# Performance work log

Hardware: AMD Instinct MI355X
Metric: run time of the kernel (lower is better)

The kernel has to match this reference:

```python
import jax, jax.numpy as jnp
import numpy as np


def conv1x1(x, w, b):
    # x: [B,Cin,H,W], w: [Cout,Cin], b: [Cout]
    return jnp.einsum('bchw,oc->bohw', x, w) + b[None, :, None, None]


def setup_inputs() -> dict:
    key = jax.random.key(0)
    ks = jax.random.split(key, 10)
    B, Cm, C, H, W = 4, 6, 64, 64, 64
    map1 = jax.random.normal(ks[0], (B, Cm, H, W), jnp.float32)
    map2 = jax.random.normal(ks[1], (B, Cm, H, W), jnp.float32)
    feature_map = jax.random.normal(ks[2], (B, C, H, W), jnp.float32)
    # 1x1 conv params (kaiming-ish scale)
    wb = jax.random.normal(ks[3], (Cm, Cm), jnp.float32) / np.sqrt(Cm)
    bb = jnp.zeros((Cm,), jnp.float32)
    wc = jax.random.normal(ks[4], (Cm, Cm), jnp.float32) / np.sqrt(Cm)
    bc = jnp.zeros((Cm,), jnp.float32)
    wd = jax.random.normal(ks[5], (C, C), jnp.float32) / np.sqrt(C)
    bd = jnp.zeros((C,), jnp.float32)
    alpha = jnp.zeros((1,), jnp.float32)
    return {"map1": map1, "map2": map2, "feature_map": feature_map,
            "wb": wb, "bb": bb, "wc": wc, "bc": bc, "wd": wd, "bd": bd,
            "alpha": alpha}


def reference(map1, map2, feature_map, wb, bb, wc, bc, wd, bd, alpha):
    B, _, H, W = map1.shape
    N = H * W
    # conv1x1 projections, flatten spatial
    feat_b = conv1x1(map1, wb, bb).reshape(B, -1, N).transpose(0, 2, 1)  # [B,N,6]
    feat_c = conv1x1(map2, wc, bc).reshape(B, -1, N)                      # [B,6,N]
    attention_s = jax.nn.softmax(jnp.einsum('bnc,bcm->bnm', feat_b, feat_c), axis=-1)  # [B,N,N]
    feat_d = conv1x1(feature_map, wd, bd).reshape(B, -1, N)               # [B,C,N]
    # bmm with attention_s^T: out[b,c,n] = sum_m feat_d[b,c,m] * attn[b,n,m]
    feat_e = jnp.einsum('bcm,bnm->bcn', feat_d, attention_s).reshape(B, -1, H, W)
    return alpha * feat_e + feature_map
```

## Files before the change

### kernel.cpp

```cpp
#include <hip/hip_runtime.h>
#include <hip/hip_bf16.h>
#include <math.h>


#define BATCH 4
#define CMAP  6
#define CH    64
#define NSP   4096
#define TN    64
#define NTW   16
#define PSTR  72

typedef __attribute__((ext_vector_type(8))) short short8;
typedef __attribute__((ext_vector_type(4))) float f32x4;

#if __has_builtin(__builtin_amdgcn_exp2f)
#define EXP2(x) __builtin_amdgcn_exp2f(x)
#else
#define EXP2(x) exp2f(x)
#endif

__device__ __forceinline__ unsigned f2bf(float f) {
    unsigned u = __float_as_uint(f);
    return (u + 0x7fffu + ((u >> 16) & 1u)) >> 16;
}

#define INVLN2 1.44269504088896f
#define SHIFT_BF16 0xC238u
#define ONE_BF16   0x3F80u


__global__ void proj_kernel(const float* __restrict__ map1, const float* __restrict__ map2,
                            const float* __restrict__ fm,
                            const float* __restrict__ wb, const float* __restrict__ bb,
                            const float* __restrict__ wc, const float* __restrict__ bc,
                            const float* __restrict__ wd, const float* __restrict__ bd,
                            unsigned short* __restrict__ featq8,
                            unsigned short* __restrict__ featk8,
                            unsigned short* __restrict__ featdf)
{
    __shared__ unsigned short vfrag[2048];

    const int b    = blockIdx.z;
    const int half = blockIdx.y;
    const int lane = threadIdx.x & 63;
    const int og   = threadIdx.x >> 6;
    const int n    = blockIdx.x * 64 + lane;

    const int ht = lane >> 5;
    const int mm = lane & 31;
    const int q4 = mm >> 3, jj = mm & 7;
    const int cb_local = og >> 1;
    float vals[CH];
#pragma unroll
    for (int c = 0; c < CH; ++c)
        vals[c] = fm[(size_t)(b*CH + c)*NSP + n];
#pragma unroll
    for (int oi = 0; oi < 8; ++oi) {
        const int o = half*32 + og*8 + oi;
        float a = bd[o];
#pragma unroll
        for (int c = 0; c < CH; ++c)
            a = fmaf(vals[c], wd[o*CH + c], a);
        const int r = (og & 1)*8 + oi;
        vfrag[(ht*2 + cb_local)*512 + (q4*16 + r)*8 + jj] = (unsigned short)f2bf(a);
    }

    if (half == 0 && og == 0) {
        float v1[CMAP], v2[CMAP];
#pragma unroll
        for (int c = 0; c < CMAP; ++c) {
            v1[c] = map1[(size_t)(b*CMAP + c)*NSP + n];
            v2[c] = map2[(size_t)(b*CMAP + c)*NSP + n];
        }
        unsigned qv[CMAP], kv[CMAP];
#pragma unroll
        for (int o = 0; o < CMAP; ++o) {
            float a1 = bb[o], a2 = bc[o];
#pragma unroll
            for (int c = 0; c < CMAP; ++c) {
                a1 = fmaf(v1[c], wb[o*CMAP + c], a1);
                a2 = fmaf(v2[c], wc[o*CMAP + c], a2);
            }
            qv[o] = f2bf(a1 * INVLN2);
            kv[o] = f2bf(a2);
        }
        uint4 qw, kw;
        qw.x = qv[0] | (qv[1] << 16);
        qw.y = qv[2] | (qv[3] << 16);
        qw.z = qv[4] | (qv[5] << 16);
        qw.w = SHIFT_BF16;
        kw.x = kv[0] | (kv[1] << 16);
        kw.y = kv[2] | (kv[3] << 16);
        kw.z = kv[4] | (kv[5] << 16);
        kw.w = ONE_BF16;
        *(uint4*)&featq8[(size_t)(b*NSP + n)*8] = qw;
        *(uint4*)&featk8[(size_t)(b*NSP + n)*8] = kw;
    }

    __syncthreads();

    {
        const int tt = threadIdx.x;
        const uint4 d = *(const uint4*)&vfrag[tt*8];
        const int ht2 = tt >> 7, inner = tt & 127;
        const size_t off = (((size_t)(b*128 + blockIdx.x*2 + ht2)*4) + half*2)*512
                         + (size_t)inner*8;
        *(uint4*)&featdf[off] = d;
    }
}

__global__ __launch_bounds__(256, 4)
void attn_kernel(const unsigned short* __restrict__ featq8,
                 const unsigned short* __restrict__ featk8,
                 const unsigned short* __restrict__ featdf,
                 const float* __restrict__ fm, const float* __restrict__ alpha_p,
                 float* __restrict__ out)
{
    __shared__ unsigned short p_scr[2][4][16*PSTR];
    __shared__ float cmb[3][64][20];

    const int b    = blockIdx.y;
    const int t    = threadIdx.x;
    const int lane = t & 63, w = t >> 6;
    const int row16 = lane & 15, quad = lane >> 4;
    const int n0   = blockIdx.x * 16;
    const int m0   = w * (NSP/4);

    short8 qf = {0,0,0,0,0,0,0,0};
    if (quad == 0)
        qf = *(const short8*)&featq8[(size_t)(b*NSP + n0 + row16)*8];

    const short8 onesb = {(short)ONE_BF16,(short)ONE_BF16,(short)ONE_BF16,(short)ONE_BF16,
                          (short)ONE_BF16,(short)ONE_BF16,(short)ONE_BF16,(short)ONE_BF16};

    const unsigned short* kbase = featk8 + ((size_t)(b*NSP + m0) + row16)*8 + quad*8;
    const unsigned short* vfb = featdf + ((size_t)b*128*4)*512 + lane*8;
    const int hb = w * 32;

    const f32x4 zf = {0.f,0.f,0.f,0.f};
    f32x4 acc[4] = {zf, zf, zf, zf};
    f32x4 accL = zf;
    const int prow = row16 * PSTR;

#define PAM_DO(pwp, mb, sv)                                                     \
    {                                                                           \
        const float p0 = EXP2(sv[0]), p1 = EXP2(sv[1]);                         \
        const float p2 = EXP2(sv[2]), p3 = EXP2(sv[3]);                         \
        uint2 pp;                                                               \
        pp.x = __builtin_amdgcn_perm(__float_as_uint(p1), __float_as_uint(p0), 0x07060302u); \
        pp.y = __builtin_amdgcn_perm(__float_as_uint(p3), __float_as_uint(p2), 0x07060302u); \
        *(uint2*)((pwp) + (mb)*16) = pp;                                        \
    }

#define LOADK(mt)                                                               \
    kc0 = *(const short8*)(kbase + ((mt)*TN +  0)*8);                           \
    kc1 = *(const short8*)(kbase + ((mt)*TN + 16)*8);                           \
    kc2 = *(const short8*)(kbase + ((mt)*TN + 32)*8);                           \
    kc3 = *(const short8*)(kbase + ((mt)*TN + 48)*8);

#define LOADV(vt)                                                               \
    vv0 = *(const short8*)(vfb + (size_t)((hb + (vt)*2 + 0)*4 + 0)*512);        \
    vv1 = *(const short8*)(vfb + (size_t)((hb + (vt)*2 + 1)*4 + 0)*512);        \
    vv2 = *(const short8*)(vfb + (size_t)((hb + (vt)*2 + 0)*4 + 1)*512);        \
    vv3 = *(const short8*)(vfb + (size_t)((hb + (vt)*2 + 1)*4 + 1)*512);        \
    vv4 = *(const short8*)(vfb + (size_t)((hb + (vt)*2 + 0)*4 + 2)*512);        \
    vv5 = *(const short8*)(vfb + (size_t)((hb + (vt)*2 + 1)*4 + 2)*512);        \
    vv6 = *(const short8*)(vfb + (size_t)((hb + (vt)*2 + 1)*4 + 3)*512);        \
    vv7 = *(const short8*)(vfb + (size_t)((hb + (vt)*2 + 0)*4 + 3)*512);

#define PV(a0_, a1_)                                                            \
    acc[0] = __builtin_amdgcn_mfma_f32_16x16x32_bf16(a0_, vv0, acc[0], 0, 0, 0); \
    acc[0] = __builtin_amdgcn_mfma_f32_16x16x32_bf16(a1_, vv1, acc[0], 0, 0, 0); \
    acc[1] = __builtin_amdgcn_mfma_f32_16x16x32_bf16(a0_, vv2, acc[1], 0, 0, 0); \
    acc[1] = __builtin_amdgcn_mfma_f32_16x16x32_bf16(a1_, vv3, acc[1], 0, 0, 0); \
    acc[2] = __builtin_amdgcn_mfma_f32_16x16x32_bf16(a0_, vv4, acc[2], 0, 0, 0); \
    acc[2] = __builtin_amdgcn_mfma_f32_16x16x32_bf16(a1_, vv5, acc[2], 0, 0, 0); \
    acc[3] = __builtin_amdgcn_mfma_f32_16x16x32_bf16(a0_, vv7, acc[3], 0, 0, 0); \
    acc[3] = __builtin_amdgcn_mfma_f32_16x16x32_bf16(a1_, vv6, acc[3], 0, 0, 0); \
    accL   = __builtin_amdgcn_mfma_f32_16x16x32_bf16(a0_, onesb, accL, 0, 0, 0); \
    accL   = __builtin_amdgcn_mfma_f32_16x16x32_bf16(a1_, onesb, accL, 0, 0, 0);

    short8 kc0, kc1, kc2, kc3;
    short8 vv0, vv1, vv2, vv3, vv4, vv5, vv6, vv7;
    f32x4 sp0, sp1, sp2, sp3;

    LOADK(0)
    {
        f32x4 a0 = __builtin_amdgcn_mfma_f32_16x16x32_bf16(kc0, qf, zf, 0, 0, 0);
        f32x4 a1 = __builtin_amdgcn_mfma_f32_16x16x32_bf16(kc1, qf, zf, 0, 0, 0);
        f32x4 a2 = __builtin_amdgcn_mfma_f32_16x16x32_bf16(kc2, qf, zf, 0, 0, 0);
        f32x4 a3 = __builtin_amdgcn_mfma_f32_16x16x32_bf16(kc3, qf, zf, 0, 0, 0);
        LOADK(1)
        unsigned short* pw = &p_scr[0][w][prow + quad*4];
        PAM_DO(pw, 0, a0) PAM_DO(pw, 1, a1) PAM_DO(pw, 2, a2) PAM_DO(pw, 3, a3)
    }
    sp0 = __builtin_amdgcn_mfma_f32_16x16x32_bf16(kc0, qf, zf, 0, 0, 0);
    sp1 = __builtin_amdgcn_mfma_f32_16x16x32_bf16(kc1, qf, zf, 0, 0, 0);
    sp2 = __builtin_amdgcn_mfma_f32_16x16x32_bf16(kc2, qf, zf, 0, 0, 0);
    sp3 = __builtin_amdgcn_mfma_f32_16x16x32_bf16(kc3, qf, zf, 0, 0, 0);
    LOADK(2)
    LOADV(0)

#pragma unroll 2
    for (int i = 2; i < NTW; ++i) {
        const f32x4 t0 = __builtin_amdgcn_mfma_f32_16x16x32_bf16(kc0, qf, zf, 0, 0, 0);
        const f32x4 t1 = __builtin_amdgcn_mfma_f32_16x16x32_bf16(kc1, qf, zf, 0, 0, 0);
        const f32x4 t2 = __builtin_amdgcn_mfma_f32_16x16x32_bf16(kc2, qf, zf, 0, 0, 0);
        const f32x4 t3 = __builtin_amdgcn_mfma_f32_16x16x32_bf16(kc3, qf, zf, 0, 0, 0);

        LOADK(i + 1)

        const unsigned short* pr = &p_scr[i & 1][w][prow + quad*8];
        const short8 a0 = *(const short8*)pr;
        const short8 a1 = *(const short8*)(pr + 32);

        {
            unsigned short* pw = &p_scr[(i + 1) & 1][w][prow + quad*4];
            PAM_DO(pw, 0, sp0) PAM_DO(pw, 1, sp1) PAM_DO(pw, 2, sp2) PAM_DO(pw, 3, sp3)
        }

        PV(a0, a1)

        LOADV(i - 1)

        sp0 = t0; sp1 = t1; sp2 = t2; sp3 = t3;
    }

    {
        const unsigned short* pr = &p_scr[0][w][prow + quad*8];
        const short8 a0 = *(const short8*)pr;
        const short8 a1 = *(const short8*)(pr + 32);
        unsigned short* pw = &p_scr[1][w][prow + quad*4];
        PAM_DO(pw, 0, sp0) PAM_DO(pw, 1, sp1) PAM_DO(pw, 2, sp2) PAM_DO(pw, 3, sp3)
        PV(a0, a1)
        LOADV(15)
    }
    {
        const unsigned short* pr = &p_scr[1][w][prow + quad*8];
        const short8 a0 = *(const short8*)pr;
        const short8 a1 = *(const short8*)(pr + 32);
        PV(a0, a1)
    }
#undef PAM_DO
#undef LOADK
#undef LOADV
#undef PV

    if (w != 0) {
        float* c = cmb[w - 1][lane];
#pragma unroll
        for (int cb = 0; cb < 4; ++cb)
            *(float4*)&c[cb*4] = (float4){acc[cb][0], acc[cb][1], acc[cb][2], acc[cb][3]};
        *(float4*)&c[16] = (float4){accL[0], accL[1], accL[2], accL[3]};
    }
    __syncthreads();
    if (w == 0) {
#pragma unroll
        for (int ww = 0; ww < 3; ++ww) {
            const float* c = cmb[ww][lane];
#pragma unroll
            for (int cb = 0; cb < 4; ++cb) {
                const float4 po = *(const float4*)&c[cb*4];
                acc[cb][0] += po.x; acc[cb][1] += po.y;
                acc[cb][2] += po.z; acc[cb][3] += po.w;
            }
            const float4 lo = *(const float4*)&c[16];
            accL[0] += lo.x; accL[1] += lo.y; accL[2] += lo.z; accL[3] += lo.w;
        }
        const float alpha = alpha_p[0];
        const float c0 = alpha / (accL[0] + 1e-30f);
        const float c1 = alpha / (accL[1] + 1e-30f);
        const float c2 = alpha / (accL[2] + 1e-30f);
        const float c3 = alpha / (accL[3] + 1e-30f);
#pragma unroll
        for (int cb = 0; cb < 4; ++cb) {
            const int ch = cb*16 + row16;
            const size_t base = (size_t)(b*CH + ch)*NSP + n0 + quad*4;
            const float4 f = *(const float4*)&fm[base];
            float4 o;
            o.x = fmaf(c0, acc[cb][0], f.x);
            o.y = fmaf(c1, acc[cb][1], f.y);
            o.z = fmaf(c2, acc[cb][2], f.z);
            o.w = fmaf(c3, acc[cb][3], f.w);
            *(float4*)&out[base] = o;
        }
    }
}

extern "C" void kernel_launch(void* const* d_in, const int* in_sizes, int n_in,
                              void* d_out, int out_size, void* d_ws, size_t ws_size,
                              hipStream_t stream)
{
    const float* map1  = (const float*)d_in[0];
    const float* map2  = (const float*)d_in[1];
    const float* fm    = (const float*)d_in[2];
    const float* wb    = (const float*)d_in[3];
    const float* bb    = (const float*)d_in[4];
    const float* wc    = (const float*)d_in[5];
    const float* bc    = (const float*)d_in[6];
    const float* wd    = (const float*)d_in[7];
    const float* bd    = (const float*)d_in[8];
    const float* alpha = (const float*)d_in[9];
    float* out = (float*)d_out;

    unsigned short* featq8 = (unsigned short*)d_ws;
    unsigned short* featk8 = featq8 + (size_t)BATCH*NSP*8;
    unsigned short* featdf = featk8 + (size_t)BATCH*NSP*8;

    proj_kernel<<<dim3(NSP/64, 2, BATCH), 256, 0, stream>>>(
        map1, map2, fm, wb, bb, wc, bc, wd, bd, featq8, featk8, featdf);
    attn_kernel<<<dim3(NSP/16, BATCH), 256, 0, stream>>>(
        featq8, featk8, featdf, fm, alpha, out);
}
```

Measured before the change: 122.1 us.

## Split attention blocks across channel halves and query pairs instead of key quarters

Reorganizes the attention kernel so each block covers 32 queries and one half of the 64 output channels, selected by a new grid dimension. Each wave now handles one 16-query subtile over half the key range, rather than a quarter of the keys for all channels. This shrinks per-wave V loads, accumulators and registers, and reduces the cross-wave LDS reduction to a single pairwise merge. The cost is that the QK^T scores and exponentials are recomputed for each channel half, roughly doubling softmax work overall.

```diff
diff --git a/kernel.cpp b/kernel.cpp
--- a/kernel.cpp
+++ b/kernel.cpp
@@ -8,7 +8,7 @@
 #define CH    64
 #define NSP   4096
 #define TN    64
-#define NTW   16
+#define NTH   32
 #define PSTR  72
 
 typedef __attribute__((ext_vector_type(8))) short short8;
@@ -118,28 +118,32 @@
                  float* __restrict__ out)
 {
     __shared__ unsigned short p_scr[2][4][16*PSTR];
-    __shared__ float cmb[3][64][20];
-
-    const int b    = blockIdx.y;
+    __shared__ float cmb[2][64][20];
+
+    const int b    = blockIdx.z;
+    const int chh  = blockIdx.y;
     const int t    = threadIdx.x;
     const int lane = t & 63, w = t >> 6;
     const int row16 = lane & 15, quad = lane >> 4;
-    const int n0   = blockIdx.x * 16;
-    const int m0   = w * (NSP/4);
+    const int qsub  = w >> 1;
+    const int khalf = w & 1;
+    const int n0w  = blockIdx.x * 32 + qsub * 16;
+    const int m0   = khalf * (NSP/2);
 
     short8 qf = {0,0,0,0,0,0,0,0};
     if (quad == 0)
-        qf = *(const short8*)&featq8[(size_t)(b*NSP + n0 + row16)*8];
+        qf = *(const short8*)&featq8[(size_t)(b*NSP + n0w + row16)*8];
 
     const short8 onesb = {(short)ONE_BF16,(short)ONE_BF16,(short)ONE_BF16,(short)ONE_BF16,
                           (short)ONE_BF16,(short)ONE_BF16,(short)ONE_BF16,(short)ONE_BF16};
 
     const unsigned short* kbase = featk8 + ((size_t)(b*NSP + m0) + row16)*8 + quad*8;
     const unsigned short* vfb = featdf + ((size_t)b*128*4)*512 + lane*8;
-    const int hb = w * 32;
+    const int hb  = khalf * 64;
+    const int cb0 = chh*2, cb1 = chh*2 + 1;
 
     const f32x4 zf = {0.f,0.f,0.f,0.f};
-    f32x4 acc[4] = {zf, zf, zf, zf};
+    f32x4 acc[2] = {zf, zf};
     f32x4 accL = zf;
     const int prow = row16 * PSTR;
 
@@ -160,29 +164,21 @@
     kc3 = *(const short8*)(kbase + ((mt)*TN + 48)*8);
 
 #define LOADV(vt)                                                               \
-    vv0 = *(const short8*)(vfb + (size_t)((hb + (vt)*2 + 0)*4 + 0)*512);        \
-    vv1 = *(const short8*)(vfb + (size_t)((hb + (vt)*2 + 1)*4 + 0)*512);        \
-    vv2 = *(const short8*)(vfb + (size_t)((hb + (vt)*2 + 0)*4 + 1)*512);        \
-    vv3 = *(const short8*)(vfb + (size_t)((hb + (vt)*2 + 1)*4 + 1)*512);        \
-    vv4 = *(const short8*)(vfb + (size_t)((hb + (vt)*2 + 0)*4 + 2)*512);        \
-    vv5 = *(const short8*)(vfb + (size_t)((hb + (vt)*2 + 1)*4 + 2)*512);        \
-    vv6 = *(const short8*)(vfb + (size_t)((hb + (vt)*2 + 1)*4 + 3)*512);        \
-    vv7 = *(const short8*)(vfb + (size_t)((hb + (vt)*2 + 0)*4 + 3)*512);
+    vv0 = *(const short8*)(vfb + (size_t)((hb + (vt)*2 + 0)*4 + cb0)*512);      \
+    vv1 = *(const short8*)(vfb + (size_t)((hb + (vt)*2 + 1)*4 + cb0)*512);      \
+    vv2 = *(const short8*)(vfb + (size_t)((hb + (vt)*2 + 0)*4 + cb1)*512);      \
+    vv3 = *(const short8*)(vfb + (size_t)((hb + (vt)*2 + 1)*4 + cb1)*512);
 
 #define PV(a0_, a1_)                                                            \
     acc[0] = __builtin_amdgcn_mfma_f32_16x16x32_bf16(a0_, vv0, acc[0], 0, 0, 0); \
     acc[0] = __builtin_amdgcn_mfma_f32_16x16x32_bf16(a1_, vv1, acc[0], 0, 0, 0); \
     acc[1] = __builtin_amdgcn_mfma_f32_16x16x32_bf16(a0_, vv2, acc[1], 0, 0, 0); \
     acc[1] = __builtin_amdgcn_mfma_f32_16x16x32_bf16(a1_, vv3, acc[1], 0, 0, 0); \
-    acc[2] = __builtin_amdgcn_mfma_f32_16x16x32_bf16(a0_, vv4, acc[2], 0, 0, 0); \
-    acc[2] = __builtin_amdgcn_mfma_f32_16x16x32_bf16(a1_, vv5, acc[2], 0, 0, 0); \
-    acc[3] = __builtin_amdgcn_mfma_f32_16x16x32_bf16(a0_, vv7, acc[3], 0, 0, 0); \
-    acc[3] = __builtin_amdgcn_mfma_f32_16x16x32_bf16(a1_, vv6, acc[3], 0, 0, 0); \
     accL   = __builtin_amdgcn_mfma_f32_16x16x32_bf16(a0_, onesb, accL, 0, 0, 0); \
     accL   = __builtin_amdgcn_mfma_f32_16x16x32_bf16(a1_, onesb, accL, 0, 0, 0);
 
     short8 kc0, kc1, kc2, kc3;
-    short8 vv0, vv1, vv2, vv3, vv4, vv5, vv6, vv7;
+    short8 vv0, vv1, vv2, vv3;
     f32x4 sp0, sp1, sp2, sp3;
 
     LOADK(0)
@@ -203,7 +199,7 @@
     LOADV(0)
 
 #pragma unroll 2
-    for (int i = 2; i < NTW; ++i) {
+    for (int i = 2; i < NTH; ++i) {
         const f32x4 t0 = __builtin_amdgcn_mfma_f32_16x16x32_bf16(kc0, qf, zf, 0, 0, 0);
         const f32x4 t1 = __builtin_amdgcn_mfma_f32_16x16x32_bf16(kc1, qf, zf, 0, 0, 0);
         const f32x4 t2 = __builtin_amdgcn_mfma_f32_16x16x32_bf16(kc2, qf, zf, 0, 0, 0);
@@ -234,7 +230,7 @@
         unsigned short* pw = &p_scr[1][w][prow + quad*4];
         PAM_DO(pw, 0, sp0) PAM_DO(pw, 1, sp1) PAM_DO(pw, 2, sp2) PAM_DO(pw, 3, sp3)
         PV(a0, a1)
-        LOADV(15)
+        LOADV(31)
     }
     {
         const unsigned short* pr = &p_scr[1][w][prow + quad*8];
@@ -247,42 +243,33 @@
 #undef LOADV
 #undef PV
 
-    if (w != 0) {
-        float* c = cmb[w - 1][lane];
-#pragma unroll
-        for (int cb = 0; cb < 4; ++cb)
+    if (khalf == 1) {
+        float* c = cmb[qsub][lane];
+#pragma unroll
+        for (int cb = 0; cb < 2; ++cb)
             *(float4*)&c[cb*4] = (float4){acc[cb][0], acc[cb][1], acc[cb][2], acc[cb][3]};
         *(float4*)&c[16] = (float4){accL[0], accL[1], accL[2], accL[3]};
     }
     __syncthreads();
-    if (w == 0) {
-#pragma unroll
-        for (int ww = 0; ww < 3; ++ww) {
-            const float* c = cmb[ww][lane];
-#pragma unroll
-            for (int cb = 0; cb < 4; ++cb) {
-                const float4 po = *(const float4*)&c[cb*4];
-                acc[cb][0] += po.x; acc[cb][1] += po.y;
-                acc[cb][2] += po.z; acc[cb][3] += po.w;
-            }
-            const float4 lo = *(const float4*)&c[16];
-            accL[0] += lo.x; accL[1] += lo.y; accL[2] += lo.z; accL[3] += lo.w;
-        }
+    if (khalf == 0) {
+        const float* c = cmb[qsub][lane];
+        const float4 lo = *(const float4*)&c[16];
         const float alpha = alpha_p[0];
-        const float c0 = alpha / (accL[0] + 1e-30f);
-        const float c1 = alpha / (accL[1] + 1e-30f);
-        const float c2 = alpha / (accL[2] + 1e-30f);
-        const float c3 = alpha / (accL[3] + 1e-30f);
-#pragma unroll
-        for (int cb = 0; cb < 4; ++cb) {
-            const int ch = cb*16 + row16;
-            const size_t base = (size_t)(b*CH + ch)*NSP + n0 + quad*4;
+        const float c0 = alpha / (accL[0] + lo.x + 1e-30f);
+        const float c1 = alpha / (accL[1] + lo.y + 1e-30f);
+        const float c2 = alpha / (accL[2] + lo.z + 1e-30f);
+        const float c3 = alpha / (accL[3] + lo.w + 1e-30f);
+#pragma unroll
+        for (int cb = 0; cb < 2; ++cb) {
+            const float4 po = *(const float4*)&c[cb*4];
+            const int ch = chh*32 + cb*16 + row16;
+            const size_t base = (size_t)(b*CH + ch)*NSP + n0w + quad*4;
             const float4 f = *(const float4*)&fm[base];
             float4 o;
-            o.x = fmaf(c0, acc[cb][0], f.x);
-            o.y = fmaf(c1, acc[cb][1], f.y);
-            o.z = fmaf(c2, acc[cb][2], f.z);
-            o.w = fmaf(c3, acc[cb][3], f.w);
+            o.x = fmaf(c0, acc[cb][0] + po.x, f.x);
+            o.y = fmaf(c1, acc[cb][1] + po.y, f.y);
+            o.z = fmaf(c2, acc[cb][2] + po.z, f.z);
+            o.w = fmaf(c3, acc[cb][3] + po.w, f.w);
             *(float4*)&out[base] = o;
         }
     }
@@ -310,6 +297,6 @@
 
     proj_kernel<<<dim3(NSP/64, 2, BATCH), 256, 0, stream>>>(
         map1, map2, fm, wb, bb, wc, bc, wd, bd, featq8, featk8, featdf);
-    attn_kernel<<<dim3(NSP/16, BATCH), 256, 0, stream>>>(
+    attn_kernel<<<dim3(NSP/32, 2, BATCH), 256, 0, stream>>>(
         featq8, featk8, featdf, fm, alpha, out);
 }
```

After: 123.9 us. Within noise of the previous version (+1.5%).
